# Optimization experiments

Measured on AMD Instinct MI355X. Metric: run time of the kernel, lower is better.

Reference implementation:

```python
import jax, jax.numpy as jnp
import numpy as np

N_QUBITS = 8
N_LAYERS = 7


def setup_inputs() -> dict:
    key = jax.random.key(0)
    ks = jax.random.split(key, 6)
    B = 65536
    return {
        "x": jax.random.normal(ks[0], (B, 2 ** N_QUBITS), dtype=jnp.float32),
        "weights": jax.random.normal(ks[1], (N_LAYERS, N_QUBITS), dtype=jnp.float32),
        "W1": jax.random.normal(ks[2], (16, 1), dtype=jnp.float32) * 0.5,
        "b1": jax.random.normal(ks[3], (16,), dtype=jnp.float32) * 0.1,
        "W2": jax.random.normal(ks[4], (1, 16), dtype=jnp.float32) * 0.5,
        "b2": jax.random.normal(ks[5], (1,), dtype=jnp.float32) * 0.1,
    }


def _apply_ry(psi, q, theta):
    # RY(theta) = [[cos(t/2), -sin(t/2)], [sin(t/2), cos(t/2)]] on wire q (axis q+1)
    c = jnp.cos(theta * 0.5)
    s = jnp.sin(theta * 0.5)
    a = jnp.take(psi, 0, axis=q + 1)
    b = jnp.take(psi, 1, axis=q + 1)
    return jnp.stack([c * a - s * b, s * a + c * b], axis=q + 1)


def _apply_cnot(psi, q):
    # CNOT control=q, target=q+1: flip target amplitudes where control=1
    ctl0 = jnp.take(psi, 0, axis=q + 1)
    ctl1 = jnp.take(psi, 1, axis=q + 1)
    # after removing axis q+1, target wire q+1 sits at axis q+1 of the slice
    ctl1 = jnp.flip(ctl1, axis=q + 1)
    return jnp.stack([ctl0, ctl1], axis=q + 1)


def _circuit(x, weights):
    B = x.shape[0]
    # AmplitudeEmbedding(normalize=True): real input -> real state (RY, CNOT are real)
    psi = x / jnp.linalg.norm(x, axis=1, keepdims=True)
    psi = psi.reshape((B,) + (2,) * N_QUBITS)  # axis 1 == wire 0 (MSB)
    for l in range(N_LAYERS):
        for q in range(N_QUBITS):
            psi = _apply_ry(psi, q, weights[l, q])
        for q in range(N_QUBITS - 1):
            psi = _apply_cnot(psi, q)
    probs = (psi ** 2).reshape(B, 2, -1)
    # <PauliZ(0)> = P(wire0=0) - P(wire0=1)
    return jnp.sum(probs[:, 0] - probs[:, 1], axis=1)


def reference(x, weights, W1, b1, W2, b2):
    z = _circuit(x, weights)[:, None]          # [B, 1]
    h = jax.nn.relu(z @ W1.T + b1)             # [B, 16]
    return jax.nn.sigmoid(h @ W2.T + b2)       # [B, 1]
```

## Files before the change

### kernel.cpp

```cpp
#include <hip/hip_runtime.h>
#include <hip/hip_bf16.h>

typedef __attribute__((ext_vector_type(8))) short bf16x8;
typedef __attribute__((ext_vector_type(4))) float f32x4;

__device__ __forceinline__ unsigned short f2bf(float f) {
    unsigned u = __builtin_bit_cast(unsigned, f);
    unsigned rnd = 0x7FFFu + ((u >> 16) & 1u);
    return (unsigned short)((u + rnd) >> 16);
}

__device__ __forceinline__ void wg_barrier() {
    asm volatile("s_waitcnt lgkmcnt(0)" ::: "memory");
    __builtin_amdgcn_sched_barrier(0);
    __builtin_amdgcn_s_barrier();
    __builtin_amdgcn_sched_barrier(0);
}

__global__ __launch_bounds__(256) void qnn_setup(const float* __restrict__ wts,
                                                 unsigned short* __restrict__ Bp) {
    __shared__ float cs[56], sn[56];
    int tid = threadIdx.x;
    if (tid < 56) {
        float th = 0.5f * wts[tid];
        cs[tid] = cosf(th);
        sn[tid] = sinf(th);
    }
    __syncthreads();

    int l = tid & 63;
    int k = blockIdx.x * 4 + (tid >> 6);
    int a0 = l << 2;

    float v0 = (float)(a0 + 0 == k);
    float v1 = (float)(a0 + 1 == k);
    float v2 = (float)(a0 + 2 == k);
    float v3 = (float)(a0 + 3 == k);

#pragma unroll
    for (int L = 0; L < 7; ++L) {
#pragma unroll
        for (int q = 0; q <= 5; ++q) {
            int m = 5 - q;
            float c = cs[L * 8 + q], s = sn[L * 8 + q];
            float ss = ((l >> m) & 1) ? s : -s;
            float p0 = __shfl_xor(v0, 1 << m);
            float p1 = __shfl_xor(v1, 1 << m);
            float p2 = __shfl_xor(v2, 1 << m);
            float p3 = __shfl_xor(v3, 1 << m);
            v0 = fmaf(ss, p0, c * v0);
            v1 = fmaf(ss, p1, c * v1);
            v2 = fmaf(ss, p2, c * v2);
            v3 = fmaf(ss, p3, c * v3);
        }
        {
            float c = cs[L * 8 + 6], s = sn[L * 8 + 6];
            float n0 = fmaf(-s, v2, c * v0), n2 = fmaf(s, v0, c * v2);
            float n1 = fmaf(-s, v3, c * v1), n3 = fmaf(s, v1, c * v3);
            v0 = n0; v1 = n1; v2 = n2; v3 = n3;
        }
        {
            float c = cs[L * 8 + 7], s = sn[L * 8 + 7];
            float n0 = fmaf(-s, v1, c * v0), n1 = fmaf(s, v0, c * v1);
            float n2 = fmaf(-s, v3, c * v2), n3 = fmaf(s, v2, c * v3);
            v0 = n0; v1 = n1; v2 = n2; v3 = n3;
        }
        {
            int src = l;
#pragma unroll
            for (int q = 4; q >= 0; --q)
                src = src ^ (((src >> (5 - q)) & 1) << (4 - q));
            v0 = __shfl(v0, src);
            v1 = __shfl(v1, src);
            v2 = __shfl(v2, src);
            v3 = __shfl(v3, src);
        }
        {
            bool cc = (l & 1);
            float n0 = cc ? v2 : v0, n2 = cc ? v0 : v2;
            float n1 = cc ? v3 : v1, n3 = cc ? v1 : v3;
            v0 = n0; v1 = n1; v2 = n2; v3 = n3;
        }
        {
            float t = v2; v2 = v3; v3 = t;
        }
    }

    int t = k >> 5, j = k & 7, lk = (k >> 3) & 3;
#pragma unroll
    for (int r = 0; r < 4; ++r) {
        int n = a0 + r;
        int u = n >> 4;
        int ls = lk * 16 + (n & 15);
        float val = (r == 0) ? v0 : (r == 1) ? v1 : (r == 2) ? v2 : v3;
        Bp[(((u * 8 + t) * 64) + ls) * 8 + j] = f2bf(val);
    }
}

__device__ __forceinline__ void cvt_store(const float4* pf,
                                          unsigned short (*Xp)[256],
                                          int sr, int qt) {
#pragma unroll
    for (int h2 = 0; h2 < 2; ++h2) {
        float4 a = pf[2 * h2], b = pf[2 * h2 + 1];
        bf16x8 h;
        h[0] = (short)f2bf(a.x); h[1] = (short)f2bf(a.y);
        h[2] = (short)f2bf(a.z); h[3] = (short)f2bf(a.w);
        h[4] = (short)f2bf(b.x); h[5] = (short)f2bf(b.y);
        h[6] = (short)f2bf(b.z); h[7] = (short)f2bf(b.w);
        int chunk = qt * 2 + h2;
        *(bf16x8*)&Xp[sr][(chunk ^ (sr & 7)) * 8] = h;
    }
}

__global__ __launch_bounds__(512, 4) void qnn_main(
    const float* __restrict__ x, const unsigned short* __restrict__ Bp,
    const float* __restrict__ W1, const float* __restrict__ b1,
    const float* __restrict__ W2, const float* __restrict__ b2,
    float* __restrict__ out) {
    __shared__ __align__(16) unsigned short Xs[2][32][256];
    __shared__ float Qpart[8][128];

    int tid = threadIdx.x;
    int l = tid & 63, w = tid >> 6;
    int sr = tid >> 4, qt = tid & 15;
    size_t base = (size_t)blockIdx.x * 128 * 256;
    const float* xst = x + base + (size_t)sr * 256 + qt * 16;

    const unsigned short* up = Bp + (size_t)(2 * w) * 4096 + l * 8;
    bf16x8 uf0[8], uf1[8];
#pragma unroll
    for (int t = 0; t < 8; ++t) {
        uf0[t] = *(const bf16x8*)(up + t * 512);
        uf1[t] = *(const bf16x8*)(up + 4096 + t * 512);
    }

    float4 pf[2][4];
#pragma unroll
    for (int i = 0; i < 4; ++i) pf[0][i] = *(const float4*)(xst + 4 * i);
#pragma unroll
    for (int i = 0; i < 4; ++i) pf[1][i] = *(const float4*)(xst + 8192 + 4 * i);
    cvt_store(pf[0], Xs[0], sr, qt);
    wg_barrier();

    int row = l & 15, kg = l >> 4;

#pragma unroll
    for (int t = 0; t < 4; ++t) {
        if (t + 2 < 4) {
#pragma unroll
            for (int i = 0; i < 4; ++i)
                pf[t & 1][i] = *(const float4*)(xst + (size_t)(t + 2) * 8192 + 4 * i);
        }
        __builtin_amdgcn_s_setprio(1);
#pragma unroll
        for (int tau = 0; tau < 2; ++tau) {
            const unsigned short* rp = &Xs[t & 1][tau * 16 + row][0];
            int rsw = (tau * 16 + row) & 7;
            f32x4 a0 = {0.f, 0.f, 0.f, 0.f}, a1 = {0.f, 0.f, 0.f, 0.f};
#pragma unroll
            for (int ks = 0; ks < 8; ++ks) {
                bf16x8 xf = *(const bf16x8*)(rp + (((ks << 2) | kg) ^ rsw) * 8);
                a0 = __builtin_amdgcn_mfma_f32_16x16x32_bf16(uf0[ks], xf, a0, 0, 0, 0);
                a1 = __builtin_amdgcn_mfma_f32_16x16x32_bf16(uf1[ks], xf, a1, 0, 0, 0);
            }
            float q = 0.f;
#pragma unroll
            for (int j = 0; j < 4; ++j)
                q = fmaf(a0[j], a0[j], fmaf(a1[j], a1[j], q));
            q += __shfl_xor(q, 16);
            q += __shfl_xor(q, 32);
            if (l < 16) Qpart[w][t * 32 + tau * 16 + l] = q;
        }
        __builtin_amdgcn_s_setprio(0);
        if (t + 1 < 4)
            cvt_store(pf[(t + 1) & 1], Xs[(t + 1) & 1], sr, qt);
        wg_barrier();
    }

    if (tid < 128) {
        float pp = Qpart[0][tid] + Qpart[1][tid] + Qpart[2][tid] + Qpart[3][tid];
        float pm = Qpart[4][tid] + Qpart[5][tid] + Qpart[6][tid] + Qpart[7][tid];
        float z = (pp - pm) / (pp + pm);
        float o = b2[0];
#pragma unroll
        for (int jj = 0; jj < 16; ++jj) {
            float h = fmaf(z, W1[jj], b1[jj]);
            h = h > 0.f ? h : 0.f;
            o = fmaf(W2[jj], h, o);
        }
        out[(size_t)blockIdx.x * 128 + tid] = 1.f / (1.f + expf(-o));
    }
}

extern "C" void kernel_launch(void* const* d_in, const int* in_sizes, int n_in,
                              void* d_out, int out_size, void* d_ws, size_t ws_size,
                              hipStream_t stream) {
    const float* x   = (const float*)d_in[0];
    const float* wts = (const float*)d_in[1];
    const float* W1  = (const float*)d_in[2];
    const float* b1  = (const float*)d_in[3];
    const float* W2  = (const float*)d_in[4];
    const float* b2  = (const float*)d_in[5];
    float* out = (float*)d_out;
    unsigned short* Bp = (unsigned short*)d_ws;

    int B = in_sizes[0] >> 8;
    qnn_setup<<<64, 256, 0, stream>>>(wts, Bp);
    qnn_main<<<B / 128, 512, 0, stream>>>(x, Bp, W1, b1, W2, b2, out);
}
```

Before: 26.81 us.

## Compute only wire-0=1 probability half and use input norm for normalization

```diff
diff --git a/kernel.cpp b/kernel.cpp
--- a/kernel.cpp
+++ b/kernel.cpp
@@ -99,10 +99,13 @@
 
 __device__ __forceinline__ void cvt_store(const float4* pf,
                                           unsigned short (*Xp)[256],
-                                          int sr, int qt) {
+                                          float* NrmT, int sr, int qt) {
+    float ss = 0.f;
 #pragma unroll
     for (int h2 = 0; h2 < 2; ++h2) {
         float4 a = pf[2 * h2], b = pf[2 * h2 + 1];
+        ss = fmaf(a.x, a.x, fmaf(a.y, a.y, fmaf(a.z, a.z, fmaf(a.w, a.w, ss))));
+        ss = fmaf(b.x, b.x, fmaf(b.y, b.y, fmaf(b.z, b.z, fmaf(b.w, b.w, ss))));
         bf16x8 h;
         h[0] = (short)f2bf(a.x); h[1] = (short)f2bf(a.y);
         h[2] = (short)f2bf(a.z); h[3] = (short)f2bf(a.w);
@@ -111,23 +114,35 @@
         int chunk = qt * 2 + h2;
         *(bf16x8*)&Xp[sr][(chunk ^ (sr & 7)) * 8] = h;
     }
-}
-
-__global__ __launch_bounds__(512, 4) void qnn_main(
+    ss += __shfl_xor(ss, 1);
+    ss += __shfl_xor(ss, 2);
+    ss += __shfl_xor(ss, 4);
+    ss += __shfl_xor(ss, 8);
+    if (qt == 0) NrmT[sr] = ss;
+}
+
+__global__ __launch_bounds__(256, 4) void qnn_main(
     const float* __restrict__ x, const unsigned short* __restrict__ Bp,
     const float* __restrict__ W1, const float* __restrict__ b1,
     const float* __restrict__ W2, const float* __restrict__ b2,
     float* __restrict__ out) {
-    __shared__ __align__(16) unsigned short Xs[2][32][256];
-    __shared__ float Qpart[8][128];
+    __shared__ __align__(16) unsigned short Xs[2][16][256];
+    __shared__ float Qpart[4][64];
+    __shared__ float Nrm[64];
 
     int tid = threadIdx.x;
     int l = tid & 63, w = tid >> 6;
     int sr = tid >> 4, qt = tid & 15;
-    size_t base = (size_t)blockIdx.x * 128 * 256;
+    size_t base = (size_t)blockIdx.x * 64 * 256;
     const float* xst = x + base + (size_t)sr * 256 + qt * 16;
 
-    const unsigned short* up = Bp + (size_t)(2 * w) * 4096 + l * 8;
+    float4 pf[2][4];
+#pragma unroll
+    for (int i = 0; i < 4; ++i) pf[0][i] = *(const float4*)(xst + 4 * i);
+#pragma unroll
+    for (int i = 0; i < 4; ++i) pf[1][i] = *(const float4*)(xst + 4096 + 4 * i);
+
+    const unsigned short* up = Bp + (size_t)(8 + 2 * w) * 4096 + l * 8;
     bf16x8 uf0[8], uf1[8];
 #pragma unroll
     for (int t = 0; t < 8; ++t) {
@@ -135,12 +150,7 @@
         uf1[t] = *(const bf16x8*)(up + 4096 + t * 512);
     }
 
-    float4 pf[2][4];
-#pragma unroll
-    for (int i = 0; i < 4; ++i) pf[0][i] = *(const float4*)(xst + 4 * i);
-#pragma unroll
-    for (int i = 0; i < 4; ++i) pf[1][i] = *(const float4*)(xst + 8192 + 4 * i);
-    cvt_store(pf[0], Xs[0], sr, qt);
+    cvt_store(pf[0], Xs[0], Nrm, sr, qt);
     wg_barrier();
 
     int row = l & 15, kg = l >> 4;
@@ -150,17 +160,14 @@
         if (t + 2 < 4) {
 #pragma unroll
             for (int i = 0; i < 4; ++i)
-                pf[t & 1][i] = *(const float4*)(xst + (size_t)(t + 2) * 8192 + 4 * i);
-        }
-        __builtin_amdgcn_s_setprio(1);
-#pragma unroll
-        for (int tau = 0; tau < 2; ++tau) {
-            const unsigned short* rp = &Xs[t & 1][tau * 16 + row][0];
-            int rsw = (tau * 16 + row) & 7;
+                pf[t & 1][i] = *(const float4*)(xst + (size_t)(t + 2) * 4096 + 4 * i);
+        }
+        {
+            const unsigned short* rp = &Xs[t & 1][row][0];
             f32x4 a0 = {0.f, 0.f, 0.f, 0.f}, a1 = {0.f, 0.f, 0.f, 0.f};
 #pragma unroll
             for (int ks = 0; ks < 8; ++ks) {
-                bf16x8 xf = *(const bf16x8*)(rp + (((ks << 2) | kg) ^ rsw) * 8);
+                bf16x8 xf = *(const bf16x8*)(rp + (((ks << 2) | kg) ^ (row & 7)) * 8);
                 a0 = __builtin_amdgcn_mfma_f32_16x16x32_bf16(uf0[ks], xf, a0, 0, 0, 0);
                 a1 = __builtin_amdgcn_mfma_f32_16x16x32_bf16(uf1[ks], xf, a1, 0, 0, 0);
             }
@@ -170,18 +177,17 @@
                 q = fmaf(a0[j], a0[j], fmaf(a1[j], a1[j], q));
             q += __shfl_xor(q, 16);
             q += __shfl_xor(q, 32);
-            if (l < 16) Qpart[w][t * 32 + tau * 16 + l] = q;
-        }
-        __builtin_amdgcn_s_setprio(0);
+            if (l < 16) Qpart[w][t * 16 + l] = q;
+        }
         if (t + 1 < 4)
-            cvt_store(pf[(t + 1) & 1], Xs[(t + 1) & 1], sr, qt);
+            cvt_store(pf[(t + 1) & 1], Xs[(t + 1) & 1],
+                      Nrm + (t + 1) * 16, sr, qt);
         wg_barrier();
     }
 
-    if (tid < 128) {
-        float pp = Qpart[0][tid] + Qpart[1][tid] + Qpart[2][tid] + Qpart[3][tid];
-        float pm = Qpart[4][tid] + Qpart[5][tid] + Qpart[6][tid] + Qpart[7][tid];
-        float z = (pp - pm) / (pp + pm);
+    if (tid < 64) {
+        float pm = Qpart[0][tid] + Qpart[1][tid] + Qpart[2][tid] + Qpart[3][tid];
+        float z = 1.f - 2.f * pm / Nrm[tid];
         float o = b2[0];
 #pragma unroll
         for (int jj = 0; jj < 16; ++jj) {
@@ -189,7 +195,7 @@
             h = h > 0.f ? h : 0.f;
             o = fmaf(W2[jj], h, o);
         }
-        out[(size_t)blockIdx.x * 128 + tid] = 1.f / (1.f + expf(-o));
+        out[(size_t)blockIdx.x * 64 + tid] = 1.f / (1.f + expf(-o));
     }
 }
 
@@ -207,5 +213,5 @@
 
     int B = in_sizes[0] >> 8;
     qnn_setup<<<64, 256, 0, stream>>>(wts, Bp);
-    qnn_main<<<B / 128, 512, 0, stream>>>(x, Bp, W1, b1, W2, b2, out);
-}
+    qnn_main<<<B / 64, 256, 0, stream>>>(x, Bp, W1, b1, W2, b2, out);
+}
```

Measured after the change: 27.70 us. 1.03x slower.
